# Kernel optimization log

Hardware: AMD Instinct MI355X
Metric: run time of the kernel (lower is better)

Reference implementation:

```python
import jax, jax.numpy as jnp
import numpy as np

DIM = 768      # model dim
NHEAD = 12     # heads
HD = DIM // NHEAD
SCALE = HD ** -0.5
B = 8          # batch
SPEC = 4       # spec_frames
T = 8          # num_frames // 2
AP = 196       # audio_patch (kv tokens per spec frame)
VP = 196       # vmae spatial patches (q tokens per frame)


def setup_inputs() -> dict:
    key = jax.random.key(0)
    ks = jax.random.split(key, 10)
    f = lambda k, sh: jax.random.normal(k, sh, dtype=jnp.float32)
    return {
        "s_x": f(ks[0], (AP, B * SPEC, DIM)),
        "t_x": f(ks[1], (1 + VP, B * T, DIM)),
        "clip_space_pos": SCALE * f(ks[2], (AP, DIM)),
        "clip_temporal_pos": SCALE * f(ks[3], (SPEC, DIM)),
        "vmae_space_pos": SCALE * f(ks[4], (VP, DIM)),
        "vmae_temporal_pos": SCALE * f(ks[5], (T, DIM)),
        "Wq": 0.02 * f(ks[6], (DIM, DIM)),
        "q_bias": jnp.zeros((DIM,), jnp.float32),
        "Wkv": 0.02 * f(ks[7], (2 * DIM, DIM)),
        "kv_bias": jnp.zeros((2 * DIM,), jnp.float32),
        "Wproj": 0.02 * f(ks[8], (DIM, DIM)),
        "proj_bias": jnp.zeros((DIM,), jnp.float32),
    }


def reference(s_x, t_x, clip_space_pos, clip_temporal_pos, vmae_space_pos,
              vmae_temporal_pos, Wq, q_bias, Wkv, kv_bias, Wproj, proj_bias):
    # attn_all_frame=True path of CrossAttentionS2T.s2t_cross_attn
    t_cls, t_pat = t_x[:1], t_x[1:]

    # s_x: (n, b*st, d) -> b st n d, + space pos; -> b n st d, + temporal pos; -> b (n st) d
    s = s_x.reshape(AP, B, SPEC, DIM).transpose(1, 2, 0, 3) + clip_space_pos
    s = s.transpose(0, 2, 1, 3) + clip_temporal_pos
    s = s.reshape(B, AP * SPEC, DIM)

    # t_x_pat: (n, b*t, d) -> b t n d, + space pos; -> b n t d, + temporal pos; -> b (n t) d
    q_in = t_pat.reshape(VP, B, T, DIM).transpose(1, 2, 0, 3) + vmae_space_pos
    q_in = q_in.transpose(0, 2, 1, 3) + vmae_temporal_pos
    q_in = q_in.reshape(B, VP * T, DIM)

    # Q projection: [B, Nq, D] -> [B, H, Nq, hd], pre-scaled
    q = (q_in @ Wq.T + q_bias).reshape(B, VP * T, NHEAD, HD).transpose(0, 2, 1, 3) * SCALE
    # KV projection: [B, Nk, 2D] -> split (e h d) order
    kv = (s @ Wkv.T + kv_bias).reshape(B, AP * SPEC, 2, NHEAD, HD)
    k = kv[:, :, 0].transpose(0, 2, 1, 3)  # [B, H, Nk, hd]
    v = kv[:, :, 1].transpose(0, 2, 1, 3)

    attn = jax.nn.softmax(jnp.einsum('bhqd,bhkd->bhqk', q, k), axis=-1)
    o = jnp.einsum('bhqk,bhkd->bhqd', attn, v)
    o = o.transpose(0, 2, 1, 3).reshape(B, VP * T, DIM)
    o = o @ Wproj.T + proj_bias

    # 'b (n t) d -> n (b t) d'
    o = o.reshape(B, VP, T, DIM).transpose(1, 0, 2, 3).reshape(VP, B * T, DIM)
    return jnp.concatenate([t_cls, o], axis=0)
```

## Files before the change

kernel.cpp:

```cpp
#include <hip/hip_runtime.h>
#include <stdint.h>

#define DIM 768
#define NHEAD 12
#define HD 64
#define B_ 8
#define SPEC 4
#define T_ 8
#define AP 196
#define VP 196
#define MQ (VP*T_)
#define NKV (AP*SPEC)
#define QSCALE 0.1803368801111618f

typedef short bf16x8 __attribute__((ext_vector_type(8)));
typedef short bf16x4 __attribute__((ext_vector_type(4)));
typedef float f32x4 __attribute__((ext_vector_type(4)));

__device__ __forceinline__ ushort f2bf(float f) {
    union { float f; unsigned u; } v; v.f = f;
    unsigned u = v.u;
    return (ushort)((u + 0x7fffu + ((u >> 16) & 1u)) >> 16);
}

__device__ __forceinline__ float fexp2(float x) {
    float r;
    asm("v_exp_f32 %0, %1" : "=v"(r) : "v"(x));
    return r;
}

__device__ __forceinline__ unsigned pk2(float a, float b) {
    union { float f; unsigned u; } ua, ub; ua.f = a; ub.f = b;
    return (ub.u & 0xFFFF0000u) | (ua.u >> 16);
}

typedef const __attribute__((address_space(1))) void GV;
typedef __attribute__((address_space(3))) void LV;
__device__ __forceinline__ void gload16(const void* g, void* l) {
    __builtin_amdgcn_global_load_lds((GV*)g, (LV*)l, 16, 0, 0);
}


__global__ void prep_all_k(const float* __restrict__ t_x,
                           const float* __restrict__ vsp,
                           const float* __restrict__ vtp,
                           const float* __restrict__ s_x,
                           const float* __restrict__ csp,
                           const float* __restrict__ ctp,
                           const float* __restrict__ Wq,
                           const float* __restrict__ Wkv,
                           const float* __restrict__ Wpj,
                           ushort* __restrict__ qin,
                           ushort* __restrict__ sb,
                           ushort* __restrict__ wqb,
                           ushort* __restrict__ wkvb,
                           ushort* __restrict__ wpjb,
                           float* __restrict__ out) {
    int bid = blockIdx.x;
    if (bid < 9408) {
        int i = bid * 256 + threadIdx.x;
        int d4 = i % (DIM / 4);
        int rest = i / (DIM / 4);
        int m = rest % MQ;
        int b = rest / MQ;
        int vp = m >> 3, t = m & 7;
        const float4 a  = *(const float4*)(t_x + ((size_t)(1 + vp) * (B_ * T_) + b * T_ + t) * DIM + d4 * 4);
        const float4 p1 = *(const float4*)(vsp + (size_t)vp * DIM + d4 * 4);
        const float4 p2 = *(const float4*)(vtp + (size_t)t * DIM + d4 * 4);
        ushort4 r;
        r.x = f2bf(a.x + p1.x + p2.x);
        r.y = f2bf(a.y + p1.y + p2.y);
        r.z = f2bf(a.z + p1.z + p2.z);
        r.w = f2bf(a.w + p1.w + p2.w);
        *(ushort4*)(qin + ((size_t)(b * MQ + m)) * DIM + d4 * 4) = r;
    } else if (bid < 14112) {
        int i = (bid - 9408) * 256 + threadIdx.x;
        int d4 = i % (DIM / 4);
        int rest = i / (DIM / 4);
        int n = rest % NKV;
        int b = rest / NKV;
        int ap = n >> 2, spec = n & 3;
        const float4 a  = *(const float4*)(s_x + ((size_t)ap * (B_ * SPEC) + b * SPEC + spec) * DIM + d4 * 4);
        const float4 p1 = *(const float4*)(csp + (size_t)ap * DIM + d4 * 4);
        const float4 p2 = *(const float4*)(ctp + (size_t)spec * DIM + d4 * 4);
        ushort4 r;
        r.x = f2bf(a.x + p1.x + p2.x);
        r.y = f2bf(a.y + p1.y + p2.y);
        r.z = f2bf(a.z + p1.z + p2.z);
        r.w = f2bf(a.w + p1.w + p2.w);
        *(ushort4*)(sb + ((size_t)(b * NKV + n)) * DIM + d4 * 4) = r;
    } else if (bid < 16416) {
        const float* src; ushort* dst; int i;
        if (bid < 14688)      { src = Wq;  dst = wqb;  i = (bid - 14112) * 256 + threadIdx.x; }
        else if (bid < 15840) { src = Wkv; dst = wkvb; i = (bid - 14688) * 256 + threadIdx.x; }
        else                  { src = Wpj; dst = wpjb; i = (bid - 15840) * 256 + threadIdx.x; }
        float4 v = *(const float4*)(src + (size_t)i * 4);
        ushort4 r;
        r.x = f2bf(v.x); r.y = f2bf(v.y); r.z = f2bf(v.z); r.w = f2bf(v.w);
        *(ushort4*)(dst + (size_t)i * 4) = r;
    } else {
        int i = (bid - 16416) * 256 + threadIdx.x;
        *(float4*)(out + (size_t)i * 4) = *(const float4*)(t_x + (size_t)i * 4);
    }
}


template <int MODE>
__device__ __forceinline__ void gemm_body(ushort* As, ushort* Bs,
                                          const ushort* __restrict__ A,
                                          const ushort* __restrict__ Bw,
                                          const float* __restrict__ bias,
                                          ushort* __restrict__ out_a,
                                          ushort* __restrict__ out_b,
                                          float* __restrict__ out_f,
                                          int m0, int n0) {
    const int tid = threadIdx.x;
    const int lane = tid & 63, wid = tid >> 6;
    const int wm = wid >> 1, wn = wid & 1;
    const int lr = lane & 15, hi = lane >> 4;

    const int srow = wid * 32 + (lane >> 2);
    const int scolb = (lane & 3) * 16;
    const char* gA = (const char*)A + ((size_t)(m0 + srow) * DIM) * 2 + scolb;
    const char* gB = (const char*)Bw + ((size_t)(n0 + srow) * DIM) * 2 + scolb;
    const size_t radv = (size_t)16 * DIM * 2;
    char* lA = (char*)As + wid * 2048;
    char* lB = (char*)Bs + wid * 2048;

    f32x4 acc[4][4] = {};

    for (int k0 = 0; k0 < DIM; k0 += 32) {
        size_t ko = (size_t)k0 * 2;
        gload16(gA + ko,        lA);
        gload16(gA + ko + radv, lA + 1024);
        gload16(gB + ko,        lB);
        gload16(gB + ko + radv, lB + 1024);
        __syncthreads();
        bf16x8 af[4], bfr[4];
#pragma unroll
        for (int x = 0; x < 4; ++x) {
            af[x]  = *(const bf16x8*)&As[(wm * 64 + x * 16 + lr) * 32 + hi * 8];
            bfr[x] = *(const bf16x8*)&Bs[(wn * 64 + x * 16 + lr) * 32 + hi * 8];
        }
#pragma unroll
        for (int mi = 0; mi < 4; ++mi)
#pragma unroll
            for (int ni = 0; ni < 4; ++ni)
                acc[mi][ni] = __builtin_amdgcn_mfma_f32_16x16x32_bf16(af[mi], bfr[ni], acc[mi][ni], 0, 0, 0);
        __syncthreads();
    }

#pragma unroll
    for (int mi = 0; mi < 4; ++mi) {
#pragma unroll
        for (int ni = 0; ni < 4; ++ni) {
            int gn = n0 + wn * 64 + ni * 16 + lr;
            float bv = bias[gn];
            if (MODE == 1 && gn >= DIM) {
                int o2 = gn - DIM;
                int hh = o2 >> 6, d = o2 & 63;
                int gm0 = m0 + wm * 64 + mi * 16 + hi * 4;
                int b = gm0 / NKV, n = gm0 % NKV;
                ushort4 pk;
                pk.x = f2bf(acc[mi][ni][0] + bv);
                pk.y = f2bf(acc[mi][ni][1] + bv);
                pk.z = f2bf(acc[mi][ni][2] + bv);
                pk.w = f2bf(acc[mi][ni][3] + bv);
                *(ushort4*)&out_b[(((size_t)(b * NHEAD + hh)) * HD + d) * NKV + n] = pk;
                continue;
            }
#pragma unroll
            for (int r = 0; r < 4; ++r) {
                int gm = m0 + wm * 64 + mi * 16 + hi * 4 + r;
                float val = acc[mi][ni][r] + bv;
                if (MODE == 0) {
                    int b = gm / MQ, m = gm % MQ;
                    int hh = gn >> 6, d = gn & 63;
                    out_a[(((size_t)(b * NHEAD + hh)) * MQ + m) * HD + d] = f2bf(val * QSCALE);
                } else if (MODE == 1) {
                    int b = gm / NKV, n = gm % NKV;
                    int hh = gn >> 6, d = gn & 63;
                    out_a[(((size_t)(b * NHEAD + hh)) * NKV + n) * HD + d] = f2bf(val);
                } else {
                    int b = gm / MQ, m = gm % MQ;
                    int vp = m >> 3, tt = m & 7;
                    out_f[((size_t)(1 + vp) * (B_ * T_) + b * T_ + tt) * DIM + gn] = val;
                }
            }
        }
    }
}

__global__ __launch_bounds__(256) void gemm_qkv_k(const ushort* __restrict__ qin,
                                                  const ushort* __restrict__ sbuf,
                                                  const ushort* __restrict__ wqb,
                                                  const ushort* __restrict__ wkvb,
                                                  const float* __restrict__ qb,
                                                  const float* __restrict__ kvb,
                                                  ushort* __restrict__ qs,
                                                  ushort* __restrict__ kb,
                                                  ushort* __restrict__ vtb) {
    __shared__ __align__(16) ushort As[128 * 32];
    __shared__ __align__(16) ushort Bs[128 * 32];
    int bid = blockIdx.x;
    if (bid < 588) {
        int by = bid / 6, bx = bid % 6;
        gemm_body<0>(As, Bs, qin, wqb, qb, qs, nullptr, nullptr, by * 128, bx * 128);
    } else {
        int b2 = bid - 588;
        int by = b2 / 12, bx = b2 % 12;
        gemm_body<1>(As, Bs, sbuf, wkvb, kvb, kb, vtb, nullptr, by * 128, bx * 128);
    }
}

__global__ __launch_bounds__(256) void gemm_proj_k(const ushort* __restrict__ ob,
                                                   const ushort* __restrict__ wpjb,
                                                   const float* __restrict__ pjb,
                                                   float* __restrict__ out) {
    __shared__ __align__(16) ushort As[128 * 32];
    __shared__ __align__(16) ushort Bs[128 * 32];
    gemm_body<2>(As, Bs, ob, wpjb, pjb, nullptr, nullptr, out, blockIdx.y * 128, blockIdx.x * 128);
}


template <int NT>
__device__ __forceinline__ void attn_wave(const ushort* __restrict__ q,
                                          const ushort* __restrict__ kp,
                                          const ushort* __restrict__ vtp,
                                          ushort* __restrict__ obuf,
                                          int bh, int b, int h, int m0, int lane) {
    const int lr = lane & 15, hi = lane >> 4;

    bf16x8 qa0[NT], qa1[NT];
#pragma unroll
    for (int t = 0; t < NT; ++t) {
        const ushort* qp = q + ((size_t)bh * MQ + m0 + t * 16 + lr) * HD;
        qa0[t] = *(const bf16x8*)(qp + hi * 8);
        qa1[t] = *(const bf16x8*)(qp + 32 + hi * 8);
    }

    f32x4 oacc[NT][4] = {};
    float lsum[NT] = {};

    bf16x8 kA[4], kB[4];
    bf16x4 vAa[4], vAb[4], vBa[4], vBb[4];
    {
        const ushort* ka = kp + (size_t)lr * HD + hi * 8;
        kA[0] = *(const bf16x8*)ka;
        kA[1] = *(const bf16x8*)(ka + 32);
        const ushort* k2 = ka + 16 * HD;
        kA[2] = *(const bf16x8*)k2;
        kA[3] = *(const bf16x8*)(k2 + 32);
#pragma unroll
        for (int db = 0; db < 4; ++db) {
            const ushort* vp = vtp + (size_t)(db * 16 + lr) * NKV + hi * 4;
            vAa[db] = *(const bf16x4*)vp;
            vAb[db] = *(const bf16x4*)(vp + 16);
        }
    }

    auto gbody = [&](bf16x8* kc, bf16x4* vca, bf16x4* vcb,
                     bf16x8* kn, bf16x4* vna, bf16x4* vnb, int g) {
        const int nb = g * 32;
        const int np = nb + 32;
        const int npB = (np + 16 > 768) ? 768 : np + 16;
        {
            const ushort* ka = kp + (size_t)(np + lr) * HD + hi * 8;
            kn[0] = *(const bf16x8*)ka;
            kn[1] = *(const bf16x8*)(ka + 32);
            const ushort* k2 = kp + (size_t)(npB + lr) * HD + hi * 8;
            kn[2] = *(const bf16x8*)k2;
            kn[3] = *(const bf16x8*)(k2 + 32);
        }
#pragma unroll
        for (int db = 0; db < 4; ++db) {
            const ushort* vp = vtp + (size_t)(db * 16 + lr) * NKV + np + hi * 4;
            vna[db] = *(const bf16x4*)vp;
            vnb[db] = *(const bf16x4*)(vp + 16);
        }
        __builtin_amdgcn_s_setprio(1);
#pragma unroll
        for (int t = 0; t < NT; ++t) {
            f32x4 sA = {}, sB = {};
            sA = __builtin_amdgcn_mfma_f32_16x16x32_bf16(kc[0], qa0[t], sA, 0, 0, 0);
            sA = __builtin_amdgcn_mfma_f32_16x16x32_bf16(kc[1], qa1[t], sA, 0, 0, 0);
            sB = __builtin_amdgcn_mfma_f32_16x16x32_bf16(kc[2], qa0[t], sB, 0, 0, 0);
            sB = __builtin_amdgcn_mfma_f32_16x16x32_bf16(kc[3], qa1[t], sB, 0, 0, 0);
            float eA0 = fexp2(sA[0]), eA1 = fexp2(sA[1]), eA2 = fexp2(sA[2]), eA3 = fexp2(sA[3]);
            float eB0 = fexp2(sB[0]), eB1 = fexp2(sB[1]), eB2 = fexp2(sB[2]), eB3 = fexp2(sB[3]);
            lsum[t] += ((eA0 + eA1) + (eA2 + eA3)) + ((eB0 + eB1) + (eB2 + eB3));
            union { uint4 w; bf16x8 v; } pk;
            pk.w.x = pk2(eA0, eA1);
            pk.w.y = pk2(eA2, eA3);
            pk.w.z = pk2(eB0, eB1);
            pk.w.w = pk2(eB2, eB3);
#pragma unroll
            for (int db = 0; db < 4; ++db) {
                union { struct { bf16x4 lo, hi_; } s; bf16x8 v; } vf;
                vf.s.lo = vca[db]; vf.s.hi_ = vcb[db];
                oacc[t][db] = __builtin_amdgcn_mfma_f32_16x16x32_bf16(pk.v, vf.v, oacc[t][db], 0, 0, 0);
            }
        }
        __builtin_amdgcn_s_setprio(0);
    };

    for (int gp = 0; gp < 24; gp += 2) {
        gbody(kA, vAa, vAb, kB, vBa, vBb, gp);
        gbody(kB, vBa, vBb, kA, vAa, vAb, gp + 1);
    }

    {
#pragma unroll
        for (int t = 0; t < NT; ++t) {
            f32x4 sA = {};
            sA = __builtin_amdgcn_mfma_f32_16x16x32_bf16(kA[0], qa0[t], sA, 0, 0, 0);
            sA = __builtin_amdgcn_mfma_f32_16x16x32_bf16(kA[1], qa1[t], sA, 0, 0, 0);
            float eA0 = fexp2(sA[0]), eA1 = fexp2(sA[1]), eA2 = fexp2(sA[2]), eA3 = fexp2(sA[3]);
            lsum[t] += (eA0 + eA1) + (eA2 + eA3);
            union { uint4 w; bf16x8 v; } pk;
            pk.w.x = pk2(eA0, eA1);
            pk.w.y = pk2(eA2, eA3);
            pk.w.z = 0;
            pk.w.w = 0;
#pragma unroll
            for (int db = 0; db < 4; ++db) {
                union { struct { bf16x4 lo, hi_; } s; bf16x8 v; } vf;
                vf.s.lo = vAa[db]; vf.s.hi_ = vAa[db];
                oacc[t][db] = __builtin_amdgcn_mfma_f32_16x16x32_bf16(pk.v, vf.v, oacc[t][db], 0, 0, 0);
            }
        }
    }

#pragma unroll
    for (int t = 0; t < NT; ++t) {
        float sum = lsum[t];
        sum += __shfl_xor(sum, 16);
        sum += __shfl_xor(sum, 32);
        float inv = 1.0f / sum;
#pragma unroll
        for (int r = 0; r < 4; ++r) {
            float invr = __shfl(inv, hi * 4 + r);
            int m = m0 + t * 16 + hi * 4 + r;
            ushort* op = obuf + ((size_t)b * MQ + m) * DIM + h * HD;
#pragma unroll
            for (int db = 0; db < 4; ++db)
                op[db * 16 + lr] = f2bf(oacc[t][db][r] * invr);
        }
    }
}

__global__ __launch_bounds__(128) void attn_k(const ushort* __restrict__ q,
                                              const ushort* __restrict__ kbuf,
                                              const ushort* __restrict__ vt,
                                              ushort* __restrict__ obuf) {
    const int lane = threadIdx.x & 63, wid = threadIdx.x >> 6;
    const int bid = blockIdx.x;
    const int bh = bid % 96;
    const int mb = bid / 96;
    const int b = bh / NHEAD, h = bh % NHEAD;
    const ushort* kp  = kbuf + (size_t)bh * NKV * HD;
    const ushort* vtp = vt + (size_t)bh * HD * NKV;
    const int mbase = mb * 112;
    if (wid == 0)
        attn_wave<4>(q, kp, vtp, obuf, bh, b, h, mbase, lane);
    else
        attn_wave<3>(q, kp, vtp, obuf, bh, b, h, mbase + 64, lane);
}


extern "C" void kernel_launch(void* const* d_in, const int* in_sizes, int n_in,
                              void* d_out, int out_size, void* d_ws, size_t ws_size,
                              hipStream_t stream) {
    const float* s_x  = (const float*)d_in[0];
    const float* t_x  = (const float*)d_in[1];
    const float* csp  = (const float*)d_in[2];
    const float* ctp  = (const float*)d_in[3];
    const float* vsp  = (const float*)d_in[4];
    const float* vtp  = (const float*)d_in[5];
    const float* Wq   = (const float*)d_in[6];
    const float* qb   = (const float*)d_in[7];
    const float* Wkv  = (const float*)d_in[8];
    const float* kvb  = (const float*)d_in[9];
    const float* Wpj  = (const float*)d_in[10];
    const float* pjb  = (const float*)d_in[11];
    float* out = (float*)d_out;

    ushort* w = (ushort*)d_ws;
    ushort* qin  = w; w += (size_t)B_ * MQ * DIM;
    ushort* sb   = w; w += (size_t)B_ * NKV * DIM;
    ushort* wqb  = w; w += (size_t)DIM * DIM;
    ushort* wkvb = w; w += (size_t)2 * DIM * DIM;
    ushort* wpjb = w; w += (size_t)DIM * DIM;
    ushort* qs   = w; w += (size_t)B_ * NHEAD * MQ * HD;
    ushort* kb   = w; w += (size_t)B_ * NHEAD * NKV * HD;
    ushort* vtb  = w; w += (size_t)B_ * NHEAD * HD * NKV;
    ushort* ob   = w; w += (size_t)B_ * MQ * DIM;

    prep_all_k<<<16464, 256, 0, stream>>>(t_x, vsp, vtp, s_x, csp, ctp,
                                          Wq, Wkv, Wpj,
                                          qin, sb, wqb, wkvb, wpjb, out);

    gemm_qkv_k<<<588 + 588, 256, 0, stream>>>(qin, sb, wqb, wkvb, qb, kvb, qs, kb, vtb);

    attn_k<<<1344, 128, 0, stream>>>(qs, kb, vtb, ob);

    gemm_proj_k<<<dim3(DIM / 128, B_ * MQ / 128), 256, 0, stream>>>(ob, wpjb, pjb, out);
}
```

Measured before the change: 166.1 us.

## Split attention KV range across wave pairs and merge partial sums in LDS

Measured after the change: 180.2 us. 8.5% more time.

```diff
diff --git a/kernel.cpp b/kernel.cpp
--- a/kernel.cpp
+++ b/kernel.cpp
@@ -224,11 +224,12 @@
 
 
 template <int NT>
-__device__ __forceinline__ void attn_wave(const ushort* __restrict__ q,
-                                          const ushort* __restrict__ kp,
-                                          const ushort* __restrict__ vtp,
-                                          ushort* __restrict__ obuf,
-                                          int bh, int b, int h, int m0, int lane) {
+__device__ __forceinline__ void attn_compute(const ushort* __restrict__ q,
+                                             const ushort* __restrict__ kp,
+                                             const ushort* __restrict__ vtp,
+                                             int bh, int m0, int lane,
+                                             int gstart, int gend, int dotail,
+                                             f32x4 (*oacc)[4], float* lsum) {
     const int lr = lane & 15, hi = lane >> 4;
 
     bf16x8 qa0[NT], qa1[NT];
@@ -239,13 +240,11 @@
         qa1[t] = *(const bf16x8*)(qp + 32 + hi * 8);
     }
 
-    f32x4 oacc[NT][4] = {};
-    float lsum[NT] = {};
-
     bf16x8 kA[4], kB[4];
     bf16x4 vAa[4], vAb[4], vBa[4], vBb[4];
     {
-        const ushort* ka = kp + (size_t)lr * HD + hi * 8;
+        const int nb0 = gstart * 32;
+        const ushort* ka = kp + (size_t)(nb0 + lr) * HD + hi * 8;
         kA[0] = *(const bf16x8*)ka;
         kA[1] = *(const bf16x8*)(ka + 32);
         const ushort* k2 = ka + 16 * HD;
@@ -253,7 +252,7 @@
         kA[3] = *(const bf16x8*)(k2 + 32);
 #pragma unroll
         for (int db = 0; db < 4; ++db) {
-            const ushort* vp = vtp + (size_t)(db * 16 + lr) * NKV + hi * 4;
+            const ushort* vp = vtp + (size_t)(db * 16 + lr) * NKV + nb0 + hi * 4;
             vAa[db] = *(const bf16x4*)vp;
             vAb[db] = *(const bf16x4*)(vp + 16);
         }
@@ -304,12 +303,12 @@
         __builtin_amdgcn_s_setprio(0);
     };
 
-    for (int gp = 0; gp < 24; gp += 2) {
+    for (int gp = gstart; gp < gend; gp += 2) {
         gbody(kA, vAa, vAb, kB, vBa, vBb, gp);
         gbody(kB, vBa, vBb, kA, vAa, vAb, gp + 1);
     }
 
-    {
+    if (dotail) {
 #pragma unroll
         for (int t = 0; t < NT; ++t) {
             f32x4 sA = {};
@@ -330,41 +329,74 @@
             }
         }
     }
-
-#pragma unroll
-    for (int t = 0; t < NT; ++t) {
-        float sum = lsum[t];
-        sum += __shfl_xor(sum, 16);
-        sum += __shfl_xor(sum, 32);
-        float inv = 1.0f / sum;
-#pragma unroll
-        for (int r = 0; r < 4; ++r) {
-            float invr = __shfl(inv, hi * 4 + r);
-            int m = m0 + t * 16 + hi * 4 + r;
-            ushort* op = obuf + ((size_t)b * MQ + m) * DIM + h * HD;
-#pragma unroll
-            for (int db = 0; db < 4; ++db)
-                op[db * 16 + lr] = f2bf(oacc[t][db][r] * invr);
-        }
-    }
-}
-
-__global__ __launch_bounds__(128) void attn_k(const ushort* __restrict__ q,
+}
+
+__global__ __launch_bounds__(256) void attn_k(const ushort* __restrict__ q,
                                               const ushort* __restrict__ kbuf,
                                               const ushort* __restrict__ vt,
                                               ushort* __restrict__ obuf) {
+    __shared__ f32x4 cO[2][4][4][64];
+    __shared__ float cL[2][4][64];
     const int lane = threadIdx.x & 63, wid = threadIdx.x >> 6;
+    const int pair = wid >> 1, half = wid & 1;
     const int bid = blockIdx.x;
     const int bh = bid % 96;
     const int mb = bid / 96;
     const int b = bh / NHEAD, h = bh % NHEAD;
     const ushort* kp  = kbuf + (size_t)bh * NKV * HD;
     const ushort* vtp = vt + (size_t)bh * HD * NKV;
-    const int mbase = mb * 112;
-    if (wid == 0)
-        attn_wave<4>(q, kp, vtp, obuf, bh, b, h, mbase, lane);
+    const int m0 = mb * 112 + pair * 64;
+    const int NTr = pair ? 3 : 4;
+
+    f32x4 oacc[4][4] = {};
+    float lsum[4] = {};
+    const int gstart = half ? 12 : 0;
+    const int gend   = half ? 24 : 12;
+    if (pair == 0)
+        attn_compute<4>(q, kp, vtp, bh, m0, lane, gstart, gend, half, oacc, lsum);
     else
-        attn_wave<3>(q, kp, vtp, obuf, bh, b, h, mbase + 64, lane);
+        attn_compute<3>(q, kp, vtp, bh, m0, lane, gstart, gend, half, oacc, lsum);
+
+    if (half) {
+#pragma unroll
+        for (int t = 0; t < 4; ++t) {
+            if (t >= NTr) break;
+#pragma unroll
+            for (int db = 0; db < 4; ++db)
+                cO[pair][t][db][lane] = oacc[t][db];
+            cL[pair][t][lane] = lsum[t];
+        }
+    }
+    __syncthreads();
+    if (half) return;
+
+#pragma unroll
+    for (int t = 0; t < 4; ++t) {
+        if (t >= NTr) break;
+#pragma unroll
+        for (int db = 0; db < 4; ++db)
+            oacc[t][db] += cO[pair][t][db][lane];
+        lsum[t] += cL[pair][t][lane];
+    }
+
+    const int lr = lane & 15, hi = lane >> 4;
+#pragma unroll
+    for (int t = 0; t < 4; ++t) {
+        if (t >= NTr) break;
+        float sum = lsum[t];
+        sum += __shfl_xor(sum, 16);
+        sum += __shfl_xor(sum, 32);
+        float inv = 1.0f / sum;
+#pragma unroll
+        for (int r = 0; r < 4; ++r) {
+            float invr = __shfl(inv, hi * 4 + r);
+            int m = m0 + t * 16 + hi * 4 + r;
+            ushort* op = obuf + ((size_t)b * MQ + m) * DIM + h * HD;
+#pragma unroll
+            for (int db = 0; db < 4; ++db)
+                op[db * 16 + lr] = f2bf(oacc[t][db][r] * invr);
+        }
+    }
 }
 
 
@@ -402,7 +434,7 @@
 
     gemm_qkv_k<<<588 + 588, 256, 0, stream>>>(qin, sb, wqb, wkvb, qb, kvb, qs, kb, vtb);
 
-    attn_k<<<1344, 128, 0, stream>>>(qs, kb, vtb, ob);
+    attn_k<<<1344, 256, 0, stream>>>(qs, kb, vtb, ob);
 
     gemm_proj_k<<<dim3(DIM / 128, B_ * MQ / 128), 256, 0, stream>>>(ob, wpjb, pjb, out);
 }
```
